# Optimization experiments

Measured on AMD Instinct MI355X. Metric: run time of the kernel, lower is better.

## Reference

```python
import jax, jax.numpy as jnp
import numpy as np

N, E = 50000, 800000
NFEAT, NHID, NCLASS = 512, 256, 64
RRELU_SLOPE = (1.0 / 8.0 + 1.0 / 3.0) / 2.0  # nn.RReLU eval-mode negative slope


def spmm(row, col, val, X):
    # sparse adj (COO: row, col, val) @ dense X -> [N, F]
    return jax.ops.segment_sum(X[col] * val[:, None], row, num_segments=N)


def setup_inputs() -> dict:
    key = jax.random.key(0)
    ks = jax.random.split(key, 12)
    x = jax.random.normal(ks[0], (N, NFEAT), dtype=jnp.float32)
    edge_row = jnp.sort(jax.random.randint(ks[1], (E,), 0, N))
    edge_col = jax.random.randint(ks[2], (E,), 0, N)
    # normalized-ish positive adjacency values
    edge_val = jax.random.uniform(ks[3], (E,), dtype=jnp.float32) / 16.0
    def glorot(k, fi, fo):
        s = 1.0 / np.sqrt(fi)
        return jax.random.normal(k, (fi, fo), dtype=jnp.float32) * s
    w1 = glorot(ks[4], NFEAT, NHID)
    b1 = jax.random.normal(ks[5], (NHID,), dtype=jnp.float32) * 0.01
    w2 = glorot(ks[6], NFEAT, NHID)
    b2 = jax.random.normal(ks[7], (NHID,), dtype=jnp.float32) * 0.01
    w3 = glorot(ks[8], NHID, NCLASS)
    b3 = jax.random.normal(ks[9], (NCLASS,), dtype=jnp.float32) * 0.01
    w4 = glorot(ks[10], NFEAT, NCLASS)
    b4 = jax.random.normal(ks[11], (NCLASS,), dtype=jnp.float32) * 0.01
    return {"x": x, "edge_row": edge_row, "edge_col": edge_col, "edge_val": edge_val,
            "w1": w1, "b1": b1, "w2": w2, "b2": b2, "w3": w3, "b3": b3, "w4": w4, "b4": b4}


def reference(x, edge_row, edge_col, edge_val, w1, b1, w2, b2, w3, b3, w4, b4):
    # skip branches (no adj): support = x @ W + b; dropout is identity in eval
    a_skip0 = x @ w2 + b2                                   # [N, NHID]
    a_skip1 = x @ w4 + b4                                   # [N, NCLASS]
    # gc1 with adj
    h1 = spmm(edge_row, edge_col, edge_val, x @ w1) + b1    # [N, NHID]
    v = h1 + a_skip0
    h = jnp.where(v >= 0, v, v * RRELU_SLOPE)               # RReLU (eval mode)
    # gc3 with adj
    out = spmm(edge_row, edge_col, edge_val, h @ w3) + b3 + a_skip1  # [N, NCLASS]
    return (out, w1, w2, w3, w4)
```

## Files before the change

kernel.cpp:

```cpp
#include <hip/hip_runtime.h>

#define N_NODES 50000
#define N_EDGES 800000
#define NFEAT 512
#define NHID 256
#define NCLASS 64
#define NCOMB 576
#define NPAD 640
#define NSKIP 320
#define RRELU_SLOPE 0.2291666666666667f

typedef __attribute__((ext_vector_type(8))) short bf16x8;
typedef __attribute__((ext_vector_type(4))) float f32x4;

#define GLOAD_LDS16(g, l)                                                      \
    __builtin_amdgcn_global_load_lds(                                          \
        (const __attribute__((address_space(1))) void*)(g),                    \
        (__attribute__((address_space(3))) void*)(l), 16, 0, 0)

__device__ __forceinline__ unsigned short f2bf(float f) {
    unsigned int x = __float_as_uint(f);
    unsigned int r = (x + 0x7fffu + ((x >> 16) & 1u)) >> 16;
    return (unsigned short)r;
}
__device__ __forceinline__ float bf2f(unsigned short u) {
    return __uint_as_float(((unsigned int)u) << 16);
}
__device__ __forceinline__ float bf_lo(unsigned int u) { return __uint_as_float(u << 16); }
__device__ __forceinline__ float bf_hi(unsigned int u) { return __uint_as_float(u & 0xffff0000u); }

#define S0 6400000
#define S1 7200000
#define S2 7527680
#define S3 7577681
#define S4 7594065
#define S5 7594705
#define S6 7672529
#define PREP_BLOCKS ((S6 + 255) / 256)

__global__ __launch_bounds__(256)
void prep(const float* __restrict__ x, const int* __restrict__ erow,
          const int* __restrict__ ecol, const float* __restrict__ ev,
          const float* __restrict__ w1, const float* __restrict__ b1,
          const float* __restrict__ w2, const float* __restrict__ b2,
          const float* __restrict__ w3, const float* __restrict__ b3,
          const float* __restrict__ w4, const float* __restrict__ b4,
          unsigned short* __restrict__ xb, unsigned short* __restrict__ Bt,
          float* __restrict__ biasb, unsigned short* __restrict__ w3t,
          uint2* __restrict__ ep, int* __restrict__ rp,
          float* __restrict__ out) {
    int i = blockIdx.x * 256 + threadIdx.x;
    if (i >= S6) return;
    if (i < S0) {
        float4 v = ((const float4*)x)[i];
        ushort4 o;
        o.x = f2bf(v.x); o.y = f2bf(v.y); o.z = f2bf(v.z); o.w = f2bf(v.w);
        ((ushort4*)xb)[i] = o;
    } else if (i < S1) {
        int j = i - S0;
        uint2 e;
        e.x = (unsigned)ecol[j];
        e.y = __float_as_uint(ev[j]);
        ep[j] = e;
    } else if (i < S2) {
        int j = i - S1;
        int c = j >> 9;
        int k = j & 511;
        float v = 0.f;
        if (c < NHID)            v = w1[k * NHID + c];
        else if (c < 2 * NHID)   v = w2[k * NHID + (c - NHID)];
        else if (c < NCOMB)      v = w4[k * NCLASS + (c - 2 * NHID)];
        Bt[j] = f2bf(v);
    } else if (i < S3) {
        int n = i - S2;
        int lo = 0, hi = N_EDGES;
        while (lo < hi) {
            int mid = (lo + hi) >> 1;
            if (erow[mid] < n) lo = mid + 1; else hi = mid;
        }
        rp[n] = lo;
    } else if (i < S4) {
        int j = i - S3;
        int c = j >> 8;
        int k = j & 255;
        w3t[j] = f2bf(w3[k * NCLASS + c]);
    } else if (i < S5) {
        int b = i - S4;
        float v = 0.f;
        if (b >= NHID && b < 2 * NHID)      v = b1[b - NHID] + b2[b - NHID];
        else if (b >= 2 * NHID && b < NCOMB) v = b3[b - 2 * NHID] + b4[b - 2 * NHID];
        biasb[b] = v;
    } else {
        int j = i - S5;
        float4* o4 = (float4*)out;
        if (j < 32768)        o4[800000 + j] = ((const float4*)w1)[j];
        else if (j < 65536)   o4[832768 + (j - 32768)] = ((const float4*)w2)[j - 32768];
        else if (j < 69632)   o4[865536 + (j - 65536)] = ((const float4*)w3)[j - 65536];
        else                  o4[869632 + (j - 69632)] = ((const float4*)w4)[j - 69632];
    }
}

#define GBM 128
#define GBK 64
#define NCB0 5
#define NRP0 392

template <int BN, int MODE>
__global__ __launch_bounds__(256)
void gemm_bf16(const unsigned short* __restrict__ A,
               const unsigned short* __restrict__ Bt,
               const float* __restrict__ bias,
               unsigned short* __restrict__ Cout,
               unsigned short* __restrict__ skipb,
               unsigned short* __restrict__ xw1b,
               int M, int K, int NC) {
    constexpr int CF = BN / 32;
    __shared__ unsigned short As[GBM * GBK];
    __shared__ unsigned short Bs[BN * GBK];
    int row0, col0;
    if (MODE == 0) {
        int b = blockIdx.x;
        int g = b / (8 * NCB0);
        int w = b % (8 * NCB0);
        int r = g * 8 + (w & 7);
        int c = w >> 3;
        if (r * GBM >= M) return;
        row0 = r * GBM;
        col0 = c * BN;
    } else {
        col0 = blockIdx.x * BN;
        row0 = blockIdx.y * GBM;
    }
    const int tid  = threadIdx.x;
    const int lane = tid & 63;
    const int wave = tid >> 6;
    const int wr = (wave >> 1) * 64;
    const int wc = (wave & 1) * (BN / 2);
    const int lm = lane & 15;
    const int l4 = lane >> 4;
    const int sw = lm & 7;

    const int sub  = lane >> 3;
    const int slot = lane & 7;
    const int goct = slot ^ sub;

    f32x4 acc[4][CF] = {};

    for (int k0 = 0; k0 < K; k0 += GBK) {
        #pragma unroll
        for (int p = 0; p < 4; ++p) {
            int chunk = wave * 4 + p;
            int gr = row0 + chunk * 8 + sub;
            if (gr > M - 1) gr = M - 1;
            GLOAD_LDS16(A + (size_t)gr * K + k0 + goct * 8, As + chunk * 512);
        }
        #pragma unroll
        for (int p = 0; p < BN / 32; ++p) {
            int chunk = wave * (BN / 32) + p;
            int rb = col0 + chunk * 8 + sub;
            GLOAD_LDS16(Bt + (size_t)rb * K + k0 + goct * 8, Bs + chunk * 512);
        }
        __syncthreads();

        #pragma unroll
        for (int kk8 = 0; kk8 < GBK / 8; kk8 += 4) {
            const int so = ((kk8 + l4) ^ sw) * 8;
            bf16x8 bfr[CF];
            #pragma unroll
            for (int j = 0; j < CF; ++j)
                bfr[j] = *(const bf16x8*)(Bs + (wc + j * 16 + lm) * 64 + so);
            #pragma unroll
            for (int i = 0; i < 4; ++i) {
                bf16x8 af = *(const bf16x8*)(As + (wr + i * 16 + lm) * 64 + so);
                #pragma unroll
                for (int j = 0; j < CF; ++j)
                    acc[i][j] = __builtin_amdgcn_mfma_f32_16x16x32_bf16(af, bfr[j], acc[i][j], 0, 0, 0);
            }
        }
        __syncthreads();
    }

    #pragma unroll
    for (int i = 0; i < 4; ++i) {
        #pragma unroll
        for (int j = 0; j < CF; ++j) {
            int col = col0 + wc + j * 16 + lm;
            float bvv = (MODE == 0) ? bias[col] : 0.f;
            #pragma unroll
            for (int r = 0; r < 4; ++r) {
                int row = row0 + wr + i * 16 + l4 * 4 + r;
                if (row < M) {
                    float v = acc[i][j][r];
                    if (MODE == 0) {
                        if (col < NHID)       xw1b[(size_t)row * NHID + col] = f2bf(v);
                        else if (col < NCOMB) skipb[(size_t)row * NSKIP + (col - NHID)] = f2bf(v + bvv);
                    } else {
                        Cout[(size_t)row * NC + col] = f2bf(v);
                    }
                }
            }
        }
    }
}

__global__ __launch_bounds__(256)
void spmm1_rrelu(const int* __restrict__ rp, const uint2* __restrict__ ep,
                 const unsigned short* __restrict__ xw1b,
                 const unsigned short* __restrict__ skipb,
                 unsigned short* __restrict__ hb, int n_nodes) {
    int n = blockIdx.x * 4 + (threadIdx.x >> 6);
    if (n >= n_nodes) return;
    int lane = threadIdx.x & 63;
    int f = lane * 4;
    int lo = rp[n], hi = rp[n + 1];
    float s0 = 0.f, s1 = 0.f, s2 = 0.f, s3 = 0.f;
    int e = lo;
    for (; e + 7 < hi; e += 8) {
        uint2 ed[8], p[8];
        #pragma unroll
        for (int q = 0; q < 8; ++q) ed[q] = ep[e + q];
        #pragma unroll
        for (int q = 0; q < 8; ++q)
            p[q] = *(const uint2*)(xw1b + (size_t)ed[q].x * NHID + f);
        #pragma unroll
        for (int q = 0; q < 8; ++q) {
            float v = __uint_as_float(ed[q].y);
            s0 += v * bf_lo(p[q].x);
            s1 += v * bf_hi(p[q].x);
            s2 += v * bf_lo(p[q].y);
            s3 += v * bf_hi(p[q].y);
        }
    }
    for (; e < hi; ++e) {
        uint2 ee = ep[e];
        float v = __uint_as_float(ee.y);
        uint2 p = *(const uint2*)(xw1b + (size_t)ee.x * NHID + f);
        s0 += v * bf_lo(p.x);
        s1 += v * bf_hi(p.x);
        s2 += v * bf_lo(p.y);
        s3 += v * bf_hi(p.y);
    }
    ushort4 sk = *(const ushort4*)(skipb + (size_t)n * NSKIP + f);
    float v0 = s0 + bf2f(sk.x), v1 = s1 + bf2f(sk.y);
    float v2 = s2 + bf2f(sk.z), v3 = s3 + bf2f(sk.w);
    v0 = (v0 >= 0.f) ? v0 : v0 * RRELU_SLOPE;
    v1 = (v1 >= 0.f) ? v1 : v1 * RRELU_SLOPE;
    v2 = (v2 >= 0.f) ? v2 : v2 * RRELU_SLOPE;
    v3 = (v3 >= 0.f) ? v3 : v3 * RRELU_SLOPE;
    ushort4 o;
    o.x = f2bf(v0); o.y = f2bf(v1); o.z = f2bf(v2); o.w = f2bf(v3);
    *(ushort4*)(hb + (size_t)n * NHID + f) = o;
}

__global__ __launch_bounds__(256)
void spmm2_out(const int* __restrict__ rp, const uint2* __restrict__ ep,
               const unsigned short* __restrict__ hw3b,
               const unsigned short* __restrict__ skipb,
               float* __restrict__ out, int n_nodes) {
    int n = blockIdx.x * 4 + (threadIdx.x >> 6);
    if (n >= n_nodes) return;
    int lane = threadIdx.x & 63;
    int half = lane >> 5;
    int fl = (lane & 31) * 2;
    int lo = rp[n], hi = rp[n + 1];
    float s0 = 0.f, s1 = 0.f;
    int e = lo + half;
    for (; e + 6 < hi; e += 8) {
        uint2 e0 = ep[e], e1 = ep[e + 2], e2 = ep[e + 4], e3 = ep[e + 6];
        unsigned p0 = *(const unsigned*)(hw3b + (size_t)e0.x * NCLASS + fl);
        unsigned p1 = *(const unsigned*)(hw3b + (size_t)e1.x * NCLASS + fl);
        unsigned p2 = *(const unsigned*)(hw3b + (size_t)e2.x * NCLASS + fl);
        unsigned p3 = *(const unsigned*)(hw3b + (size_t)e3.x * NCLASS + fl);
        float v0 = __uint_as_float(e0.y), v1 = __uint_as_float(e1.y);
        float v2 = __uint_as_float(e2.y), v3 = __uint_as_float(e3.y);
        s0 += v0 * bf_lo(p0) + v1 * bf_lo(p1) + v2 * bf_lo(p2) + v3 * bf_lo(p3);
        s1 += v0 * bf_hi(p0) + v1 * bf_hi(p1) + v2 * bf_hi(p2) + v3 * bf_hi(p3);
    }
    for (; e < hi; e += 2) {
        uint2 ee = ep[e];
        unsigned p = *(const unsigned*)(hw3b + (size_t)ee.x * NCLASS + fl);
        float v = __uint_as_float(ee.y);
        s0 += v * bf_lo(p);
        s1 += v * bf_hi(p);
    }
    s0 += __shfl_xor(s0, 32);
    s1 += __shfl_xor(s1, 32);
    if (half == 0) {
        unsigned sv = *(const unsigned*)(skipb + (size_t)n * NSKIP + NHID + fl);
        float2 o;
        o.x = s0 + bf_lo(sv);
        o.y = s1 + bf_hi(sv);
        *(float2*)(out + (size_t)n * NCLASS + fl) = o;
    }
}

extern "C" void kernel_launch(void* const* d_in, const int* in_sizes, int n_in,
                              void* d_out, int out_size, void* d_ws, size_t ws_size,
                              hipStream_t stream) {
    const float* x    = (const float*)d_in[0];
    const int*   erow = (const int*)d_in[1];
    const int*   ecol = (const int*)d_in[2];
    const float* ev   = (const float*)d_in[3];
    const float* w1   = (const float*)d_in[4];
    const float* b1   = (const float*)d_in[5];
    const float* w2   = (const float*)d_in[6];
    const float* b2   = (const float*)d_in[7];
    const float* w3   = (const float*)d_in[8];
    const float* b3   = (const float*)d_in[9];
    const float* w4   = (const float*)d_in[10];
    const float* b4   = (const float*)d_in[11];
    float* out = (float*)d_out;

    char* ws = (char*)d_ws;
    size_t off = 0;
    auto alloc = [&](size_t bytes) -> void* {
        off = (off + 255) & ~(size_t)255;
        void* p = ws + off;
        off += bytes;
        return p;
    };

    unsigned short* xb    = (unsigned short*)alloc((size_t)N_NODES * NFEAT * 2);
    unsigned short* Bt    = (unsigned short*)alloc((size_t)NFEAT * NPAD * 2);
    float*          biasb = (float*)alloc(NPAD * 4);
    unsigned short* xw1b  = (unsigned short*)alloc((size_t)N_NODES * NHID * 2);
    unsigned short* skipb = (unsigned short*)alloc((size_t)N_NODES * NSKIP * 2);
    unsigned short* hb    = (unsigned short*)alloc((size_t)N_NODES * NHID * 2);
    unsigned short* w3t   = (unsigned short*)alloc((size_t)NHID * NCLASS * 2);
    unsigned short* hw3b  = (unsigned short*)alloc((size_t)N_NODES * NCLASS * 2);
    int*            rp    = (int*)alloc((size_t)(N_NODES + 1) * 4);
    uint2*          ep    = (uint2*)alloc((size_t)N_EDGES * 8);

    prep<<<PREP_BLOCKS, 256, 0, stream>>>(x, erow, ecol, ev, w1, b1, w2, b2, w3, b3,
                                          w4, b4, xb, Bt, biasb, w3t, ep, rp, out);

    gemm_bf16<128, 0><<<NRP0 * NCB0, 256, 0, stream>>>(xb, Bt, biasb, nullptr, skipb, xw1b,
                                                       N_NODES, NFEAT, NPAD);

    spmm1_rrelu<<<(N_NODES + 3) / 4, 256, 0, stream>>>(rp, ep, xw1b, skipb, hb, N_NODES);

    dim3 g2(NCLASS / 64, (N_NODES + GBM - 1) / GBM);
    gemm_bf16<64, 1><<<g2, 256, 0, stream>>>(hb, w3t, nullptr, hw3b, nullptr, nullptr,
                                             N_NODES, NHID, NCLASS);

    spmm2_out<<<(N_NODES + 3) / 4, 256, 0, stream>>>(rp, ep, hw3b, skipb, out, N_NODES);
}
```

Measured before the change: 340.0 us.

## Store gathered SpMM operands as FP8 to halve gather traffic

The GEMM epilogues now write x@w1 and h@w3 as FP8 (e4m3) bytes instead of bf16, and both SpMM kernels gather 4-byte FP8 chunks and unpack them with hardware cvt_pk_f32_fp8. The aim is to halve the bytes moved by the random row gathers that dominate SpMM cost. spmm2 is also reorganised so four edge groups of 16 lanes each cover 4 features, reduced with two shuffles. The GEMM gets an occupancy hint through launch_bounds. FP8 carries only about 3 mantissa bits, so accuracy drops noticeably and may fail the tolerance.

```diff
diff --git a/kernel.cpp b/kernel.cpp
--- a/kernel.cpp
+++ b/kernel.cpp
@@ -12,6 +12,7 @@
 
 typedef __attribute__((ext_vector_type(8))) short bf16x8;
 typedef __attribute__((ext_vector_type(4))) float f32x4;
+typedef __attribute__((ext_vector_type(2))) float f32x2;
 
 #define GLOAD_LDS16(g, l)                                                      \
     __builtin_amdgcn_global_load_lds(                                          \
@@ -28,6 +29,9 @@
 }
 __device__ __forceinline__ float bf_lo(unsigned int u) { return __uint_as_float(u << 16); }
 __device__ __forceinline__ float bf_hi(unsigned int u) { return __uint_as_float(u & 0xffff0000u); }
+__device__ __forceinline__ unsigned char f2fp8(float v) {
+    return (unsigned char)__builtin_amdgcn_cvt_pk_fp8_f32(v, v, 0, false);
+}
 
 #define S0 6400000
 #define S1 7200000
@@ -87,7 +91,7 @@
     } else if (i < S5) {
         int b = i - S4;
         float v = 0.f;
-        if (b >= NHID && b < 2 * NHID)      v = b1[b - NHID] + b2[b - NHID];
+        if (b >= NHID && b < 2 * NHID)       v = b1[b - NHID] + b2[b - NHID];
         else if (b >= 2 * NHID && b < NCOMB) v = b3[b - 2 * NHID] + b4[b - 2 * NHID];
         biasb[b] = v;
     } else {
@@ -106,13 +110,12 @@
 #define NRP0 392
 
 template <int BN, int MODE>
-__global__ __launch_bounds__(256)
+__global__ __launch_bounds__(256, 4)
 void gemm_bf16(const unsigned short* __restrict__ A,
                const unsigned short* __restrict__ Bt,
                const float* __restrict__ bias,
-               unsigned short* __restrict__ Cout,
+               unsigned char* __restrict__ C8,
                unsigned short* __restrict__ skipb,
-               unsigned short* __restrict__ xw1b,
                int M, int K, int NC) {
     constexpr int CF = BN / 32;
     __shared__ unsigned short As[GBM * GBK];
@@ -192,10 +195,10 @@
                 if (row < M) {
                     float v = acc[i][j][r];
                     if (MODE == 0) {
-                        if (col < NHID)       xw1b[(size_t)row * NHID + col] = f2bf(v);
+                        if (col < NHID)       C8[(size_t)row * NHID + col] = f2fp8(v);
                         else if (col < NCOMB) skipb[(size_t)row * NSKIP + (col - NHID)] = f2bf(v + bvv);
                     } else {
-                        Cout[(size_t)row * NC + col] = f2bf(v);
+                        C8[(size_t)row * NC + col] = f2fp8(v);
                     }
                 }
             }
@@ -205,7 +208,7 @@
 
 __global__ __launch_bounds__(256)
 void spmm1_rrelu(const int* __restrict__ rp, const uint2* __restrict__ ep,
-                 const unsigned short* __restrict__ xw1b,
+                 const unsigned char* __restrict__ xw1q,
                  const unsigned short* __restrict__ skipb,
                  unsigned short* __restrict__ hb, int n_nodes) {
     int n = blockIdx.x * 4 + (threadIdx.x >> 6);
@@ -216,29 +219,34 @@
     float s0 = 0.f, s1 = 0.f, s2 = 0.f, s3 = 0.f;
     int e = lo;
     for (; e + 7 < hi; e += 8) {
-        uint2 ed[8], p[8];
+        uint2 ed[8];
+        unsigned p[8];
         #pragma unroll
         for (int q = 0; q < 8; ++q) ed[q] = ep[e + q];
         #pragma unroll
         for (int q = 0; q < 8; ++q)
-            p[q] = *(const uint2*)(xw1b + (size_t)ed[q].x * NHID + f);
+            p[q] = *(const unsigned*)(xw1q + (size_t)ed[q].x * NHID + f);
         #pragma unroll
         for (int q = 0; q < 8; ++q) {
             float v = __uint_as_float(ed[q].y);
-            s0 += v * bf_lo(p[q].x);
-            s1 += v * bf_hi(p[q].x);
-            s2 += v * bf_lo(p[q].y);
-            s3 += v * bf_hi(p[q].y);
+            f32x2 ab = __builtin_amdgcn_cvt_pk_f32_fp8((int)p[q], false);
+            f32x2 cd = __builtin_amdgcn_cvt_pk_f32_fp8((int)p[q], true);
+            s0 += v * ab.x;
+            s1 += v * ab.y;
+            s2 += v * cd.x;
+            s3 += v * cd.y;
         }
     }
     for (; e < hi; ++e) {
         uint2 ee = ep[e];
         float v = __uint_as_float(ee.y);
-        uint2 p = *(const uint2*)(xw1b + (size_t)ee.x * NHID + f);
-        s0 += v * bf_lo(p.x);
-        s1 += v * bf_hi(p.x);
-        s2 += v * bf_lo(p.y);
-        s3 += v * bf_hi(p.y);
+        unsigned p = *(const unsigned*)(xw1q + (size_t)ee.x * NHID + f);
+        f32x2 ab = __builtin_amdgcn_cvt_pk_f32_fp8((int)p, false);
+        f32x2 cd = __builtin_amdgcn_cvt_pk_f32_fp8((int)p, true);
+        s0 += v * ab.x;
+        s1 += v * ab.y;
+        s2 += v * cd.x;
+        s3 += v * cd.y;
     }
     ushort4 sk = *(const ushort4*)(skipb + (size_t)n * NSKIP + f);
     float v0 = s0 + bf2f(sk.x), v1 = s1 + bf2f(sk.y);
@@ -254,43 +262,55 @@
 
 __global__ __launch_bounds__(256)
 void spmm2_out(const int* __restrict__ rp, const uint2* __restrict__ ep,
-               const unsigned short* __restrict__ hw3b,
+               const unsigned char* __restrict__ hw3q,
                const unsigned short* __restrict__ skipb,
                float* __restrict__ out, int n_nodes) {
     int n = blockIdx.x * 4 + (threadIdx.x >> 6);
     if (n >= n_nodes) return;
     int lane = threadIdx.x & 63;
-    int half = lane >> 5;
-    int fl = (lane & 31) * 2;
+    int q = lane >> 4;
+    int l = lane & 15;
+    int f = l * 4;
     int lo = rp[n], hi = rp[n + 1];
-    float s0 = 0.f, s1 = 0.f;
-    int e = lo + half;
-    for (; e + 6 < hi; e += 8) {
-        uint2 e0 = ep[e], e1 = ep[e + 2], e2 = ep[e + 4], e3 = ep[e + 6];
-        unsigned p0 = *(const unsigned*)(hw3b + (size_t)e0.x * NCLASS + fl);
-        unsigned p1 = *(const unsigned*)(hw3b + (size_t)e1.x * NCLASS + fl);
-        unsigned p2 = *(const unsigned*)(hw3b + (size_t)e2.x * NCLASS + fl);
-        unsigned p3 = *(const unsigned*)(hw3b + (size_t)e3.x * NCLASS + fl);
-        float v0 = __uint_as_float(e0.y), v1 = __uint_as_float(e1.y);
-        float v2 = __uint_as_float(e2.y), v3 = __uint_as_float(e3.y);
-        s0 += v0 * bf_lo(p0) + v1 * bf_lo(p1) + v2 * bf_lo(p2) + v3 * bf_lo(p3);
-        s1 += v0 * bf_hi(p0) + v1 * bf_hi(p1) + v2 * bf_hi(p2) + v3 * bf_hi(p3);
-    }
-    for (; e < hi; e += 2) {
+    float s0 = 0.f, s1 = 0.f, s2 = 0.f, s3 = 0.f;
+    int e = lo + q;
+    for (; e + 4 < hi; e += 8) {
+        uint2 ea = ep[e], eb = ep[e + 4];
+        unsigned pa = *(const unsigned*)(hw3q + (size_t)ea.x * NCLASS + f);
+        unsigned pb = *(const unsigned*)(hw3q + (size_t)eb.x * NCLASS + f);
+        float va = __uint_as_float(ea.y), vb = __uint_as_float(eb.y);
+        f32x2 a0 = __builtin_amdgcn_cvt_pk_f32_fp8((int)pa, false);
+        f32x2 a1 = __builtin_amdgcn_cvt_pk_f32_fp8((int)pa, true);
+        f32x2 b0 = __builtin_amdgcn_cvt_pk_f32_fp8((int)pb, false);
+        f32x2 b1 = __builtin_amdgcn_cvt_pk_f32_fp8((int)pb, true);
+        s0 += va * a0.x + vb * b0.x;
+        s1 += va * a0.y + vb * b0.y;
+        s2 += va * a1.x + vb * b1.x;
+        s3 += va * a1.y + vb * b1.y;
+    }
+    for (; e < hi; e += 4) {
         uint2 ee = ep[e];
-        unsigned p = *(const unsigned*)(hw3b + (size_t)ee.x * NCLASS + fl);
+        unsigned p = *(const unsigned*)(hw3q + (size_t)ee.x * NCLASS + f);
         float v = __uint_as_float(ee.y);
-        s0 += v * bf_lo(p);
-        s1 += v * bf_hi(p);
-    }
-    s0 += __shfl_xor(s0, 32);
-    s1 += __shfl_xor(s1, 32);
-    if (half == 0) {
-        unsigned sv = *(const unsigned*)(skipb + (size_t)n * NSKIP + NHID + fl);
-        float2 o;
-        o.x = s0 + bf_lo(sv);
-        o.y = s1 + bf_hi(sv);
-        *(float2*)(out + (size_t)n * NCLASS + fl) = o;
+        f32x2 ab = __builtin_amdgcn_cvt_pk_f32_fp8((int)p, false);
+        f32x2 cd = __builtin_amdgcn_cvt_pk_f32_fp8((int)p, true);
+        s0 += v * ab.x;
+        s1 += v * ab.y;
+        s2 += v * cd.x;
+        s3 += v * cd.y;
+    }
+    s0 += __shfl_xor(s0, 16); s0 += __shfl_xor(s0, 32);
+    s1 += __shfl_xor(s1, 16); s1 += __shfl_xor(s1, 32);
+    s2 += __shfl_xor(s2, 16); s2 += __shfl_xor(s2, 32);
+    s3 += __shfl_xor(s3, 16); s3 += __shfl_xor(s3, 32);
+    if (q == 0) {
+        uint2 sv = *(const uint2*)(skipb + (size_t)n * NSKIP + NHID + f);
+        float4 o;
+        o.x = s0 + bf_lo(sv.x);
+        o.y = s1 + bf_hi(sv.x);
+        o.z = s2 + bf_lo(sv.y);
+        o.w = s3 + bf_hi(sv.y);
+        *(float4*)(out + (size_t)n * NCLASS + f) = o;
     }
 }
 
@@ -323,25 +343,25 @@
     unsigned short* xb    = (unsigned short*)alloc((size_t)N_NODES * NFEAT * 2);
     unsigned short* Bt    = (unsigned short*)alloc((size_t)NFEAT * NPAD * 2);
     float*          biasb = (float*)alloc(NPAD * 4);
-    unsigned short* xw1b  = (unsigned short*)alloc((size_t)N_NODES * NHID * 2);
+    unsigned char*  xw1q  = (unsigned char*)alloc((size_t)N_NODES * NHID);
     unsigned short* skipb = (unsigned short*)alloc((size_t)N_NODES * NSKIP * 2);
     unsigned short* hb    = (unsigned short*)alloc((size_t)N_NODES * NHID * 2);
     unsigned short* w3t   = (unsigned short*)alloc((size_t)NHID * NCLASS * 2);
-    unsigned short* hw3b  = (unsigned short*)alloc((size_t)N_NODES * NCLASS * 2);
+    unsigned char*  hw3q  = (unsigned char*)alloc((size_t)N_NODES * NCLASS);
     int*            rp    = (int*)alloc((size_t)(N_NODES + 1) * 4);
     uint2*          ep    = (uint2*)alloc((size_t)N_EDGES * 8);
 
     prep<<<PREP_BLOCKS, 256, 0, stream>>>(x, erow, ecol, ev, w1, b1, w2, b2, w3, b3,
                                           w4, b4, xb, Bt, biasb, w3t, ep, rp, out);
 
-    gemm_bf16<128, 0><<<NRP0 * NCB0, 256, 0, stream>>>(xb, Bt, biasb, nullptr, skipb, xw1b,
+    gemm_bf16<128, 0><<<NRP0 * NCB0, 256, 0, stream>>>(xb, Bt, biasb, xw1q, skipb,
                                                        N_NODES, NFEAT, NPAD);
 
-    spmm1_rrelu<<<(N_NODES + 3) / 4, 256, 0, stream>>>(rp, ep, xw1b, skipb, hb, N_NODES);
+    spmm1_rrelu<<<(N_NODES + 3) / 4, 256, 0, stream>>>(rp, ep, xw1q, skipb, hb, N_NODES);
 
     dim3 g2(NCLASS / 64, (N_NODES + GBM - 1) / GBM);
-    gemm_bf16<64, 1><<<g2, 256, 0, stream>>>(hb, w3t, nullptr, hw3b, nullptr, nullptr,
+    gemm_bf16<64, 1><<<g2, 256, 0, stream>>>(hb, w3t, nullptr, hw3q, nullptr,
                                              N_NODES, NHID, NCLASS);
 
-    spmm2_out<<<(N_NODES + 3) / 4, 256, 0, stream>>>(rp, ep, hw3b, skipb, out, N_NODES);
-}
+    spmm2_out<<<(N_NODES + 3) / 4, 256, 0, stream>>>(rp, ep, hw3q, skipb, out, N_NODES);
+}
```

Result: faster. 311.5 us (-8.4%).
